# Performance work log

Measured on AMD Instinct MI355X. Metric: run time of the kernel, lower is better.

Reference implementation:

```python
import jax, jax.numpy as jnp
import numpy as np

SMOOTH = 1.0
ALPHA = 0.7
BETA = 0.3
GAMMA = 4.0 / 3.0


def setup_inputs() -> dict:
    key = jax.random.key(0)
    k1, k2 = jax.random.split(key)
    inputs = jax.random.normal(k1, (8, 10, 512, 512), dtype=jnp.float32)
    targets = jax.random.randint(k2, (8, 512, 512), 0, 10, dtype=jnp.int32)
    return {"inputs": inputs, "targets": targets}


def reference(inputs, targets):
    # inputs: [B, C, H, W] logits; targets: [B, H, W] int labels, 0 = ignore.
    C = inputs.shape[1]
    # ignore_index=0: drop the background channel before softmax/argmax
    logits = inputs[:, 1:]                      # [B, C-1, H, W]
    probs = jax.nn.softmax(logits, axis=1)
    # argmax over remaining channels -> map back to original labels 1..C-1
    preds = jnp.argmax(probs, axis=1).astype(jnp.int32) + 1   # [B, H, W]

    t = targets.reshape(-1)
    p = preds.reshape(-1)
    mask = t != 0                               # drop ignore-class pixels

    # per-class confusion counts via fused histograms (classes 1..C-1)
    tp = jnp.bincount(jnp.where(mask & (p == t), t, 0), length=C)[1:]
    tgt_cnt = jnp.bincount(jnp.where(mask, t, 0), length=C)[1:]
    pred_cnt = jnp.bincount(jnp.where(mask, p, 0), length=C)[1:]

    TP = tp.astype(jnp.float32)
    FN = (tgt_cnt - tp).astype(jnp.float32)
    FP = (pred_cnt - tp).astype(jnp.float32)

    tversky = (TP + SMOOTH) / (TP + ALPHA * FN + BETA * FP + SMOOTH)
    return jnp.sum((1.0 - tversky) ** GAMMA)
```

## Files before the change

kernel.cpp:

```cpp
#include <hip/hip_runtime.h>


#define HW        262144
#define HW4       65536
#define NGROUPS   524288

__global__ __launch_bounds__(256) void ftl_hist(const float* __restrict__ inp,
                                                const int* __restrict__ tgt,
                                                unsigned int* __restrict__ cnt) {
    __shared__ unsigned int s[27];
    const int tid = threadIdx.x;
    if (tid < 27) s[tid] = 0u;
    __syncthreads();

    const float4* f4  = reinterpret_cast<const float4*>(inp);
    const int4*   t4p = reinterpret_cast<const int4*>(tgt);

    int i = blockIdx.x * blockDim.x + tid;
    const int gstride = gridDim.x * blockDim.x;

    for (; i < NGROUPS; i += gstride) {
        const int b  = i >> 16;
        const int gi = i & (HW4 - 1);
        const float4* base = f4 + (((size_t)(b * 10 + 1)) << 16) + gi;

        float4 v = base[0];
        float bv0 = v.x, bv1 = v.y, bv2 = v.z, bv3 = v.w;
        int   bc0 = 1,   bc1 = 1,   bc2 = 1,   bc3 = 1;
#pragma unroll
        for (int c = 2; c <= 9; ++c) {
            float4 w = base[((size_t)(c - 1)) << 16];
            if (w.x > bv0) { bv0 = w.x; bc0 = c; }
            if (w.y > bv1) { bv1 = w.y; bc1 = c; }
            if (w.z > bv2) { bv2 = w.z; bc2 = c; }
            if (w.w > bv3) { bv3 = w.w; bc3 = c; }
        }

        const int4 t = t4p[i];
        if (t.x) { atomicAdd(&s[9 + t.x - 1], 1u); atomicAdd(&s[18 + bc0 - 1], 1u); if (bc0 == t.x) atomicAdd(&s[t.x - 1], 1u); }
        if (t.y) { atomicAdd(&s[9 + t.y - 1], 1u); atomicAdd(&s[18 + bc1 - 1], 1u); if (bc1 == t.y) atomicAdd(&s[t.y - 1], 1u); }
        if (t.z) { atomicAdd(&s[9 + t.z - 1], 1u); atomicAdd(&s[18 + bc2 - 1], 1u); if (bc2 == t.z) atomicAdd(&s[t.z - 1], 1u); }
        if (t.w) { atomicAdd(&s[9 + t.w - 1], 1u); atomicAdd(&s[18 + bc3 - 1], 1u); if (bc3 == t.w) atomicAdd(&s[t.w - 1], 1u); }
    }

    __syncthreads();
    if (tid < 27) atomicAdd(&cnt[tid], s[tid]);
}

__global__ void ftl_final(const unsigned int* __restrict__ cnt, float* __restrict__ out) {
    if (threadIdx.x == 0 && blockIdx.x == 0) {
        double loss = 0.0;
#pragma unroll
        for (int c = 0; c < 9; ++c) {
            const double TP = (double)cnt[c];
            const double FN = (double)cnt[9 + c]  - TP;
            const double FP = (double)cnt[18 + c] - TP;
            const double tv = (TP + 1.0) / (TP + 0.7 * FN + 0.3 * FP + 1.0);
            loss += pow(1.0 - tv, 4.0 / 3.0);
        }
        out[0] = (float)loss;
    }
}

extern "C" void kernel_launch(void* const* d_in, const int* in_sizes, int n_in,
                              void* d_out, int out_size, void* d_ws, size_t ws_size,
                              hipStream_t stream) {
    const float* inp = (const float*)d_in[0];
    const int*   tgt = (const int*)d_in[1];
    unsigned int* cnt = (unsigned int*)d_ws;
    float* out = (float*)d_out;

    hipMemsetAsync(cnt, 0, 27 * sizeof(unsigned int), stream);

    ftl_hist<<<dim3(NGROUPS / 256), dim3(256), 0, stream>>>(inp, tgt, cnt);
    ftl_final<<<dim3(1), dim3(64), 0, stream>>>(cnt, out);
}
```

Measured before the change: 141.7 us.

## Replace global atomics with per-block partials and a parallel reduce kernel

Each histogram block now writes its 27 counters to a per-block slot in workspace instead of atomically adding into global counters, and the memset is removed. A new single-block reduce kernel with 27 groups of 32 lanes sums the partials by shuffle reduction, then computes the loss. The grid-stride loop is dropped, since the grid exactly covers the work at one group per thread. This removes contention from 2048 blocks atomically updating the same 27 global words, plus one memset launch, at the cost of a small extra read pass over 2048x27 partials.

```diff
diff --git a/kernel.cpp b/kernel.cpp
--- a/kernel.cpp
+++ b/kernel.cpp
@@ -1,60 +1,70 @@
 #include <hip/hip_runtime.h>
 
 
-#define HW        262144
-#define HW4       65536
-#define NGROUPS   524288
+#define HW4     65536
+#define NGROUPS 524288
+#define NBLK    2048
 
 __global__ __launch_bounds__(256) void ftl_hist(const float* __restrict__ inp,
                                                 const int* __restrict__ tgt,
-                                                unsigned int* __restrict__ cnt) {
+                                                unsigned int* __restrict__ pw) {
     __shared__ unsigned int s[27];
     const int tid = threadIdx.x;
     if (tid < 27) s[tid] = 0u;
     __syncthreads();
 
-    const float4* f4  = reinterpret_cast<const float4*>(inp);
-    const int4*   t4p = reinterpret_cast<const int4*>(tgt);
+    const int i  = blockIdx.x * 256 + tid;
+    const int b  = i >> 16;
+    const int gi = i & (HW4 - 1);
 
-    int i = blockIdx.x * blockDim.x + tid;
-    const int gstride = gridDim.x * blockDim.x;
+    const float4* base = reinterpret_cast<const float4*>(inp)
+                       + (((size_t)(b * 10 + 1)) << 16) + gi;
 
-    for (; i < NGROUPS; i += gstride) {
-        const int b  = i >> 16;
-        const int gi = i & (HW4 - 1);
-        const float4* base = f4 + (((size_t)(b * 10 + 1)) << 16) + gi;
-
-        float4 v = base[0];
-        float bv0 = v.x, bv1 = v.y, bv2 = v.z, bv3 = v.w;
-        int   bc0 = 1,   bc1 = 1,   bc2 = 1,   bc3 = 1;
+    float4 v = base[0];
+    float bv0 = v.x, bv1 = v.y, bv2 = v.z, bv3 = v.w;
+    int   bc0 = 1,   bc1 = 1,   bc2 = 1,   bc3 = 1;
 #pragma unroll
-        for (int c = 2; c <= 9; ++c) {
-            float4 w = base[((size_t)(c - 1)) << 16];
-            if (w.x > bv0) { bv0 = w.x; bc0 = c; }
-            if (w.y > bv1) { bv1 = w.y; bc1 = c; }
-            if (w.z > bv2) { bv2 = w.z; bc2 = c; }
-            if (w.w > bv3) { bv3 = w.w; bc3 = c; }
-        }
-
-        const int4 t = t4p[i];
-        if (t.x) { atomicAdd(&s[9 + t.x - 1], 1u); atomicAdd(&s[18 + bc0 - 1], 1u); if (bc0 == t.x) atomicAdd(&s[t.x - 1], 1u); }
-        if (t.y) { atomicAdd(&s[9 + t.y - 1], 1u); atomicAdd(&s[18 + bc1 - 1], 1u); if (bc1 == t.y) atomicAdd(&s[t.y - 1], 1u); }
-        if (t.z) { atomicAdd(&s[9 + t.z - 1], 1u); atomicAdd(&s[18 + bc2 - 1], 1u); if (bc2 == t.z) atomicAdd(&s[t.z - 1], 1u); }
-        if (t.w) { atomicAdd(&s[9 + t.w - 1], 1u); atomicAdd(&s[18 + bc3 - 1], 1u); if (bc3 == t.w) atomicAdd(&s[t.w - 1], 1u); }
+    for (int c = 2; c <= 9; ++c) {
+        float4 w = base[((size_t)(c - 1)) << 16];
+        if (w.x > bv0) { bv0 = w.x; bc0 = c; }
+        if (w.y > bv1) { bv1 = w.y; bc1 = c; }
+        if (w.z > bv2) { bv2 = w.z; bc2 = c; }
+        if (w.w > bv3) { bv3 = w.w; bc3 = c; }
     }
 
+    const int4 t = reinterpret_cast<const int4*>(tgt)[i];
+    if (t.x) { atomicAdd(&s[9 + t.x - 1], 1u); atomicAdd(&s[18 + bc0 - 1], 1u); if (bc0 == t.x) atomicAdd(&s[t.x - 1], 1u); }
+    if (t.y) { atomicAdd(&s[9 + t.y - 1], 1u); atomicAdd(&s[18 + bc1 - 1], 1u); if (bc1 == t.y) atomicAdd(&s[t.y - 1], 1u); }
+    if (t.z) { atomicAdd(&s[9 + t.z - 1], 1u); atomicAdd(&s[18 + bc2 - 1], 1u); if (bc2 == t.z) atomicAdd(&s[t.z - 1], 1u); }
+    if (t.w) { atomicAdd(&s[9 + t.w - 1], 1u); atomicAdd(&s[18 + bc3 - 1], 1u); if (bc3 == t.w) atomicAdd(&s[t.w - 1], 1u); }
+
     __syncthreads();
-    if (tid < 27) atomicAdd(&cnt[tid], s[tid]);
+    if (tid < 27) pw[tid * NBLK + blockIdx.x] = s[tid];
 }
 
-__global__ void ftl_final(const unsigned int* __restrict__ cnt, float* __restrict__ out) {
-    if (threadIdx.x == 0 && blockIdx.x == 0) {
+__global__ __launch_bounds__(896) void ftl_reduce(const unsigned int* __restrict__ pw,
+                                                  float* __restrict__ out) {
+    __shared__ double cs[27];
+    const int tid = threadIdx.x;
+    const int g = tid >> 5;
+    const int l = tid & 31;
+    if (g < 27) {
+        unsigned int sum = 0;
+        const unsigned int* row = pw + g * NBLK;
+#pragma unroll 8
+        for (int k = l; k < NBLK; k += 32) sum += row[k];
+#pragma unroll
+        for (int off = 16; off; off >>= 1) sum += __shfl_down(sum, off, 32);
+        if (l == 0) cs[g] = (double)sum;
+    }
+    __syncthreads();
+    if (tid == 0) {
         double loss = 0.0;
 #pragma unroll
         for (int c = 0; c < 9; ++c) {
-            const double TP = (double)cnt[c];
-            const double FN = (double)cnt[9 + c]  - TP;
-            const double FP = (double)cnt[18 + c] - TP;
+            const double TP = cs[c];
+            const double FN = cs[9 + c]  - TP;
+            const double FP = cs[18 + c] - TP;
             const double tv = (TP + 1.0) / (TP + 0.7 * FN + 0.3 * FP + 1.0);
             loss += pow(1.0 - tv, 4.0 / 3.0);
         }
@@ -67,11 +77,9 @@
                               hipStream_t stream) {
     const float* inp = (const float*)d_in[0];
     const int*   tgt = (const int*)d_in[1];
-    unsigned int* cnt = (unsigned int*)d_ws;
+    unsigned int* pw = (unsigned int*)d_ws;
     float* out = (float*)d_out;
 
-    hipMemsetAsync(cnt, 0, 27 * sizeof(unsigned int), stream);
-
-    ftl_hist<<<dim3(NGROUPS / 256), dim3(256), 0, stream>>>(inp, tgt, cnt);
-    ftl_final<<<dim3(1), dim3(64), 0, stream>>>(cnt, out);
+    ftl_hist<<<dim3(NBLK), dim3(256), 0, stream>>>(inp, tgt, pw);
+    ftl_reduce<<<dim3(1), dim3(896), 0, stream>>>(pw, out);
 }
```

After: 131.2 us. 1.08x faster.
